# Kernel tuning notes

Hardware: AMD Instinct MI355X
Metric: run time of the kernel (lower is better)

## Reference

```python
import math
import jax, jax.numpy as jnp
import numpy as np

B, L, D, H = 2, 2048, 1024, 16
HD = D // H  # 64

def setup_inputs() -> dict:
    key = jax.random.key(0)
    k1, k2, k3 = jax.random.split(key, 3)
    x = jax.random.normal(k1, (B, L, D), dtype=jnp.float32)
    Wqkv = jax.random.normal(k2, (3 * D, D), dtype=jnp.float32) * (1.0 / math.sqrt(D))
    Wo = jax.random.normal(k3, (D, D), dtype=jnp.float32) * (1.0 / math.sqrt(D))
    return {"x": x, "Wqkv": Wqkv, "Wo": Wo}

def reference(x, Wqkv, Wo):
    # QKV projection (torch Linear: y = x @ W.T), then split
    qkv = jnp.einsum('bld,ed->ble', x, Wqkv)  # [B, L, 3D]
    q, k, v = jnp.split(qkv, 3, axis=-1)
    # [B, H, L, HD]
    q = q.reshape(B, L, H, HD).transpose(0, 2, 1, 3)
    k = k.reshape(B, L, H, HD).transpose(0, 2, 1, 3)
    v = v.reshape(B, L, H, HD).transpose(0, 2, 1, 3)
    # scores; causal mask applied before the 1/sqrt(d) scale (as in source;
    # -inf is unchanged by scaling so math matches scale-then-mask)
    scores = jnp.einsum('bhqd,bhkd->bhqk', q, k)
    causal = jnp.tril(jnp.ones((L, L), dtype=bool))
    scores = jnp.where(causal, scores, -jnp.inf)
    attn = jax.nn.softmax(scores / math.sqrt(HD), axis=-1)
    out = jnp.einsum('bhqk,bhkd->bhqd', attn, v)  # [B, H, L, HD]
    out = out.transpose(0, 2, 1, 3).reshape(B, L, D)
    # output projection (dropout is identity in eval / p=0)
    return jnp.einsum('bld,ed->ble', out, Wo)
```

## Files before the change

kernel.cpp:

```cpp
#include <hip/hip_runtime.h>
#include <hip/hip_bf16.h>
#include <cstdint>
#include <cstddef>

#define B_SZ 2
#define L_SEQ 2048
#define DM 1024
#define NH 16
#define HDIM 64
#define BL (B_SZ * L_SEQ)
#define QKV_N (3 * DM)

typedef __attribute__((ext_vector_type(4))) float f32x4;
typedef __attribute__((ext_vector_type(16))) float f32x16;
typedef __attribute__((ext_vector_type(8))) short bf16x8;
typedef __attribute__((ext_vector_type(2))) unsigned int u32x2;
typedef __attribute__((ext_vector_type(4))) unsigned int u32x4;
typedef unsigned short u16;
typedef __attribute__((ext_vector_type(4))) unsigned short u16x4;

__device__ __forceinline__ float bf2f(u16 u) {
  union { unsigned int i; float f; } c; c.i = ((unsigned int)u) << 16; return c.f;
}
__device__ __forceinline__ u16 f2bf(float f) {
  union { float f; unsigned int i; } c; c.f = f;
  unsigned int r = c.i + 0x7fffu + ((c.i >> 16) & 1u);
  return (u16)(r >> 16);
}

__device__ __forceinline__ void gload_lds16(const void* g, void* l) {
  __builtin_amdgcn_global_load_lds(
      (const __attribute__((address_space(1))) void*)g,
      (__attribute__((address_space(3))) void*)l, 16, 0, 0);
}

__device__ __forceinline__ f32x16 mfma32(bf16x8 a, bf16x8 b, f32x16 c) {
  return __builtin_amdgcn_mfma_f32_32x32x16_bf16(a, b, c, 0, 0, 0);
}

__device__ __forceinline__ unsigned cvtpk(float lo, float hi) {
  unsigned r;
  asm("v_cvt_pk_bf16_f32 %0, %1, %2" : "=v"(r) : "v"(lo), "v"(hi));
  return r;
}
__device__ __forceinline__ void plswap(unsigned& a, unsigned& b) {
  asm("v_permlane32_swap_b32 %0, %1" : "+v"(a), "+v"(b));
}

template <int BASE>
__device__ __forceinline__ bf16x8 pack_bfrag(const f32x16& v) {
  unsigned a  = cvtpk(v[BASE + 0], v[BASE + 1]);
  unsigned a2 = cvtpk(v[BASE + 2], v[BASE + 3]);
  unsigned b  = cvtpk(v[BASE + 4], v[BASE + 5]);
  unsigned b2 = cvtpk(v[BASE + 6], v[BASE + 7]);
  plswap(a, b);
  plswap(a2, b2);
  u32x4 fw; fw[0] = a; fw[1] = a2; fw[2] = b; fw[3] = b2;
  return __builtin_bit_cast(bf16x8, fw);
}

#define N4_X  (BL * DM / 4)
#define N4_WQ (QKV_N * DM / 4)
#define N4_WO (DM * DM / 4)
__global__ __launch_bounds__(256) void cvt_all(
    const float* __restrict__ x, const float* __restrict__ wqkv,
    const float* __restrict__ wo, u16* __restrict__ x_bf,
    u16* __restrict__ w_bf, u16* __restrict__ wo_bf) {
  int i = blockIdx.x * blockDim.x + threadIdx.x;
  const int stride = gridDim.x * blockDim.x;
  const int total = N4_X + N4_WQ + N4_WO;
  for (; i < total; i += stride) {
    const float4* src;
    u16x4* dst;
    if (i < N4_X) {
      src = (const float4*)x + i; dst = (u16x4*)x_bf + i;
    } else if (i < N4_X + N4_WQ) {
      src = (const float4*)wqkv + (i - N4_X); dst = (u16x4*)w_bf + (i - N4_X);
    } else {
      src = (const float4*)wo + (i - N4_X - N4_WQ);
      dst = (u16x4*)wo_bf + (i - N4_X - N4_WQ);
    }
    float4 v = *src;
    u16x4 o;
    o[0] = f2bf(v.x); o[1] = f2bf(v.y); o[2] = f2bf(v.z); o[3] = f2bf(v.w);
    *dst = o;
  }
}

template <bool BF16_OUT>
__global__ __launch_bounds__(256) void gemm_bt(
    const u16* __restrict__ A, const u16* __restrict__ B,
    void* __restrict__ Cv, int M, int N, int K, int nbx) {
  __shared__ u16 As[128 * 64];
  __shared__ u16 Bs[128 * 64];
  const int tid = threadIdx.x;
  const int lane = tid & 63, w = tid >> 6;
  const int l31 = lane & 31, hi = lane >> 5;
  const int wr = w >> 1, wc = w & 1;

  const int bid = (int)blockIdx.x;
  const int swz = (bid & 7) * ((int)gridDim.x >> 3) + (bid >> 3);
  const int bm = (swz / nbx) * 128, bn = (swz % nbx) * 128;

  f32x16 acc00 = {}, acc01 = {}, acc10 = {}, acc11 = {};

  const int srow = lane >> 3;
  const int csw = ((lane & 7) ^ srow) * 8;
  const size_t abase = (size_t)(bm + w * 32 + srow) * K + csw;
  const size_t bbase = (size_t)(bn + w * 32 + srow) * K + csw;
  const int sw = l31 & 7;

  for (int k0 = 0; k0 < K; k0 += 64) {
#pragma unroll
    for (int c = 0; c < 4; ++c)
      gload_lds16(A + abase + (size_t)c * 8 * K + k0, &As[(w * 32 + c * 8) * 64]);
#pragma unroll
    for (int c = 0; c < 4; ++c)
      gload_lds16(B + bbase + (size_t)c * 8 * K + k0, &Bs[(w * 32 + c * 8) * 64]);
    __syncthreads();

#pragma unroll
    for (int ks = 0; ks < 4; ++ks) {
      const int sl = ((ks * 2 + hi) ^ sw) * 8;
      const bf16x8 a0 = *(const bf16x8*)&As[(wr * 64 + l31) * 64 + sl];
      const bf16x8 a1 = *(const bf16x8*)&As[(wr * 64 + 32 + l31) * 64 + sl];
      const bf16x8 b0 = *(const bf16x8*)&Bs[(wc * 64 + l31) * 64 + sl];
      const bf16x8 b1 = *(const bf16x8*)&Bs[(wc * 64 + 32 + l31) * 64 + sl];
      acc00 = mfma32(a0, b0, acc00);
      acc01 = mfma32(a0, b1, acc01);
      acc10 = mfma32(a1, b0, acc10);
      acc11 = mfma32(a1, b1, acc11);
    }
    __syncthreads();
  }

#define CWRITE(ACC, MI, NI)                                                    \
  {                                                                            \
    _Pragma("unroll")                                                          \
    for (int r = 0; r < 16; ++r) {                                             \
      const int row = bm + wr * 64 + (MI)*32 + (r & 3) + 8 * (r >> 2) + 4 * hi;\
      const int col = bn + wc * 64 + (NI)*32 + l31;                            \
      if (BF16_OUT)                                                            \
        ((u16*)Cv)[(size_t)row * N + col] = f2bf(ACC[r]);                      \
      else                                                                     \
        ((float*)Cv)[(size_t)row * N + col] = ACC[r];                          \
    }                                                                          \
  }
  CWRITE(acc00, 0, 0)
  CWRITE(acc01, 0, 1)
  CWRITE(acc10, 1, 0)
  CWRITE(acc11, 1, 1)
#undef CWRITE
}

__device__ const uint8_t JST[20] = {7,7,7,7, 6,6,6, 5,5,5, 4,4, 3,3, 2, 1,
                                    6, 4, 2, 0};
__device__ const uint8_t JT0[20] = {0,8,16,24, 0,8,16, 0,8,16, 0,8, 0,8, 0, 0,
                                    24, 16, 8, 0};
__device__ const uint8_t JT1[20] = {8,16,24,32, 8,16,24, 8,16,24, 8,16, 8,16, 8, 8,
                                    28, 20, 12, 4};
__device__ const uint8_t SB[8]   = {255, 255, 0, 2, 4, 7, 10, 14};
__device__ const uint8_t SCNT[8] = {1, 1, 2, 2, 3, 3, 4, 4};

__global__ __launch_bounds__(512) void attn_fused(const u16* __restrict__ qkv,
                                                  u16* __restrict__ aout,
                                                  u16* __restrict__ opart_lo,
                                                  u16* __restrict__ opart_hi,
                                                  float* __restrict__ lpart) {
  __shared__ u16 Kl[2][64 * 64];
  __shared__ u16 Vt[2][64 * 64];

  const int tid = threadIdx.x;
  const int lane = tid & 63, w = tid >> 6;
  const int l31 = lane & 31, hi = lane >> 5;
  const int id = (int)blockIdx.x;
  const int bh = id & 31, j = id >> 5;
  const int st = JST[j];
  const int t0 = JT0[j], t1 = JT1[j];
  const int b = bh >> 4, h = bh & 15;
  const u16* base = qkv + (size_t)b * L_SEQ * QKV_N;
  const int W = st * 256 + w * 32;
  const int qrow = W + l31;

  const int krow = tid >> 3;
  const int ks = tid & 7;
  const int kr7 = krow & 7;
  const u16* gpk_base = base + (size_t)krow * QKV_N + DM + h * HDIM + ks * 8;
  bf16x8 kr;

  const int vd0 = (tid & 31) * 2;
  const int vkg = tid >> 5;
  const int vge = tid & 7;
  const int vgo = (tid & 7) ^ 4;
  const u16* gpv_base = base + (size_t)(vkg * 4) * QKV_N + 2 * DM + h * HDIM + vd0;
  unsigned int vtmp[4];

  auto issue_loads = [&](int t) {
    kr = *(const bf16x8*)(gpk_base + (size_t)t * 64 * QKV_N);
    const u16* gpv = gpv_base + (size_t)t * 64 * QKV_N;
#pragma unroll
    for (int jj = 0; jj < 4; ++jj)
      vtmp[jj] = *(const unsigned int*)(gpv + (size_t)jj * QKV_N);
  };
  auto write_lds = [&](int buf) {
    *(bf16x8*)&Kl[buf][krow * 64 + ((ks ^ kr7) * 8)] = kr;
    u32x2 lo, hiw;
    lo[0]  = __builtin_amdgcn_perm(vtmp[1], vtmp[0], 0x05040100u);
    lo[1]  = __builtin_amdgcn_perm(vtmp[3], vtmp[2], 0x05040100u);
    hiw[0] = __builtin_amdgcn_perm(vtmp[1], vtmp[0], 0x07060302u);
    hiw[1] = __builtin_amdgcn_perm(vtmp[3], vtmp[2], 0x07060302u);
    *(u32x2*)&Vt[buf][vd0 * 64 + (((vkg >> 1) ^ vge) * 8) + (vkg & 1) * 4] = lo;
    *(u32x2*)&Vt[buf][(vd0 + 1) * 64 + (((vkg >> 1) ^ vgo) * 8) + (vkg & 1) * 4] = hiw;
  };

  bf16x8 bq[4];
  {
    const u16* qp = base + (size_t)qrow * QKV_N + h * HDIM + hi * 8;
#pragma unroll
    for (int dc = 0; dc < 4; ++dc) {
      bf16x8 tq = *(const bf16x8*)(qp + dc * 16);
#pragma unroll
      for (int i = 0; i < 8; ++i)
        tq[i] = (short)f2bf(bf2f((u16)tq[i]) * 0.18033688f);
      bq[dc] = tq;
    }
  }

  f32x16 acc0 = {}, acc1 = {};
  float lrow = 0.f;

  const int vg = ((l31 >> 1) & 7) ^ ((l31 & 1) << 2);
  const int lsw = l31 & 7;

  issue_loads(t0);
  write_lds(0);
  __syncthreads();

  for (int t = t0; t < t1; ++t) {
    const int cur = (t - t0) & 1;
    if (t + 1 < t1) issue_loads(t + 1);

    if (64 * t <= W + 31) {
      f32x16 s0 = {}, s1 = {};
#pragma unroll
      for (int dc = 0; dc < 4; ++dc) {
        const int sl = ((dc * 2 + hi) ^ lsw) * 8;
        const bf16x8 k0 = *(const bf16x8*)&Kl[cur][l31 * 64 + sl];
        const bf16x8 k1 = *(const bf16x8*)&Kl[cur][(32 + l31) * 64 + sl];
        s0 = mfma32(k0, bq[dc], s0);
        s1 = mfma32(k1, bq[dc], s1);
      }

      if (64 * t + 63 > W) {
#pragma unroll
        for (int r = 0; r < 16; ++r) {
          const int kg = t * 64 + (r & 3) + 8 * (r >> 2) + 4 * hi;
          if (kg > qrow) s0[r] = -1e30f;
          if (kg + 32 > qrow) s1[r] = -1e30f;
        }
      }

#pragma unroll
      for (int r = 0; r < 16; ++r) {
        s0[r] = exp2f(s0[r]);
        s1[r] = exp2f(s1[r]);
      }
      float r0 = 0.f, r1 = 0.f, r2 = 0.f, r3 = 0.f;
#pragma unroll
      for (int r = 0; r < 16; r += 4) {
        r0 += s0[r] + s0[r + 1];
        r1 += s0[r + 2] + s0[r + 3];
        r2 += s1[r] + s1[r + 1];
        r3 += s1[r + 2] + s1[r + 3];
      }
      lrow += (r0 + r1) + (r2 + r3);

      const bf16x8 pf0 = pack_bfrag<0>(s0);
      const bf16x8 pf1 = pack_bfrag<8>(s0);
      const bf16x8 pf2 = pack_bfrag<0>(s1);
      const bf16x8 pf3 = pack_bfrag<8>(s1);

#pragma unroll
      for (int c = 0; c < 4; ++c) {
        const bf16x8 pf = c == 0 ? pf0 : c == 1 ? pf1 : c == 2 ? pf2 : pf3;
        const int sl = ((c * 2 + hi) ^ vg) * 8;
        const bf16x8 va = *(const bf16x8*)&Vt[cur][l31 * 64 + sl];
        const bf16x8 vb = *(const bf16x8*)&Vt[cur][(32 + l31) * 64 + sl];
        acc0 = mfma32(va, pf, acc0);
        acc1 = mfma32(vb, pf, acc1);
      }
    }

    if (t + 1 < t1) write_lds(((t + 1) - t0) & 1);
    __syncthreads();
  }

  lrow += __shfl_xor(lrow, 32);

  if (SB[st] != 255) {
    const int c = t0 >> 3;
    const int slot = ((int)SB[st] + c) * 32 + bh;
    u16* po = slot < 512 ? opart_lo + (size_t)slot * 16384
                         : opart_hi + (size_t)(slot - 512) * 16384;
    const int q = w * 32 + l31;
#pragma unroll
    for (int i = 0; i < 16; ++i) {
      const int d0 = (i & 3) + 8 * (i >> 2) + 4 * hi;
      po[d0 * 256 + q] = f2bf(acc0[i]);
      po[(d0 + 32) * 256 + q] = f2bf(acc1[i]);
    }
    if (hi == 0) lpart[slot * 256 + q] = lrow;
  } else {
    const float inv = 1.f / lrow;
#pragma unroll
    for (int i = 0; i < 16; ++i) { acc0[i] *= inv; acc1[i] *= inv; }
    const bf16x8 of0 = pack_bfrag<0>(acc0);
    const bf16x8 of1 = pack_bfrag<8>(acc0);
    const bf16x8 of2 = pack_bfrag<0>(acc1);
    const bf16x8 of3 = pack_bfrag<8>(acc1);
    u16* op = aout + (size_t)(b * L_SEQ + qrow) * DM + h * HDIM + hi * 8;
    *(bf16x8*)(op + 0)  = of0;
    *(bf16x8*)(op + 16) = of1;
    *(bf16x8*)(op + 32) = of2;
    *(bf16x8*)(op + 48) = of3;
  }
}

__global__ __launch_bounds__(256) void attn_combine(
    const u16* __restrict__ opart_lo, const u16* __restrict__ opart_hi,
    const float* __restrict__ lpart, u16* __restrict__ aout) {
  const int gid = (int)blockIdx.x * 256 + (int)threadIdx.x;
  const int q = gid & 255;
  const int u = gid >> 8;
  const int st = 2 + (u >> 5), bh = u & 31;
  const int b = bh >> 4, h = bh & 15;
  const int nc = (int)SCNT[st];
  const int sb = (int)SB[st];

  const u16* pp[4];
  float L = 0.f;
#pragma unroll
  for (int c = 0; c < 4; ++c)
    if (c < nc) {
      const int slot = (sb + c) * 32 + bh;
      L += lpart[slot * 256 + q];
      pp[c] = slot < 512 ? opart_lo + (size_t)slot * 16384
                         : opart_hi + (size_t)(slot - 512) * 16384;
    }
  const float invl = 1.f / L;

  const int qrow = st * 256 + q;
  u16* op = aout + (size_t)(b * L_SEQ + qrow) * DM + h * HDIM;
#pragma unroll
  for (int d0 = 0; d0 < 64; d0 += 8) {
    float v[8] = {};
#pragma unroll
    for (int c = 0; c < 4; ++c)
      if (c < nc) {
#pragma unroll
        for (int jj = 0; jj < 8; ++jj)
          v[jj] += bf2f(pp[c][(d0 + jj) * 256 + q]);
      }
    u16x4 oa, ob;
#pragma unroll
    for (int jj = 0; jj < 4; ++jj) {
      oa[jj] = f2bf(v[jj] * invl);
      ob[jj] = f2bf(v[jj + 4] * invl);
    }
    *(u16x4*)(op + d0) = oa;
    *(u16x4*)(op + d0 + 4) = ob;
  }
}

extern "C" void kernel_launch(void* const* d_in, const int* in_sizes, int n_in,
                              void* d_out, int out_size, void* d_ws, size_t ws_size,
                              hipStream_t stream) {
  (void)in_sizes; (void)n_in; (void)out_size; (void)ws_size;
  const float* x = (const float*)d_in[0];
  const float* wqkv = (const float*)d_in[1];
  const float* wo = (const float*)d_in[2];

  char* ws = (char*)d_ws;
  u16* x_bf = (u16*)(ws);
  u16* w_bf = (u16*)(ws + (size_t)(8u << 20));
  u16* wo_bf = (u16*)(ws + (size_t)(14u << 20));
  u16* qkv_bf = (u16*)(ws + (size_t)(16u << 20));
  u16* ao_bf = x_bf;
  u16* opart_lo = (u16*)d_out;
  u16* opart_hi = (u16*)(ws + (size_t)(8u << 20));
  float* lpart = (float*)(ws + (size_t)(10u << 20));

  cvt_all<<<2048, 256, 0, stream>>>(x, wqkv, wo, x_bf, w_bf, wo_bf);

  gemm_bt<true><<<dim3(768), 256, 0, stream>>>(x_bf, w_bf, (void*)qkv_bf,
                                               BL, QKV_N, DM, QKV_N / 128);

  attn_fused<<<dim3(640), 512, 0, stream>>>(qkv_bf, ao_bf, opart_lo, opart_hi, lpart);
  attn_combine<<<dim3(192), 256, 0, stream>>>(opart_lo, opart_hi, lpart, ao_bf);

  gemm_bt<false><<<dim3(256), 256, 0, stream>>>(ao_bf, wo_bf, d_out,
                                                BL, DM, DM, DM / 128);
}
```

Measured before the change: 124.3 us.

## Fuse split-KV combine into attention kernel via last-block atomic counter

Removes the separate attn_combine launch and instead has the last finishing split block for each (stripe, head) combine the partial outputs, using a global atomic counter and threadfences. This aims to save a kernel launch and its tail latency. In exchange it adds a memset launch, extra syncthreads and fences in every split block, and a serialized combine tail run by one block per group.

Measured after the change: 260.5 us. 2.1x slower.

```diff
diff --git a/kernel.cpp b/kernel.cpp
--- a/kernel.cpp
+++ b/kernel.cpp
@@ -166,9 +166,11 @@
                                                   u16* __restrict__ aout,
                                                   u16* __restrict__ opart_lo,
                                                   u16* __restrict__ opart_hi,
-                                                  float* __restrict__ lpart) {
+                                                  float* __restrict__ lpart,
+                                                  int* __restrict__ cnt) {
   __shared__ u16 Kl[2][64 * 64];
   __shared__ u16 Vt[2][64 * 64];
+  __shared__ int lastFlag;
 
   const int tid = threadIdx.x;
   const int lane = tid & 63, w = tid >> 6;
@@ -299,7 +301,9 @@
 
   if (SB[st] != 255) {
     const int c = t0 >> 3;
-    const int slot = ((int)SB[st] + c) * 32 + bh;
+    const int sb = (int)SB[st];
+    const int nc = (int)SCNT[st];
+    const int slot = (sb + c) * 32 + bh;
     u16* po = slot < 512 ? opart_lo + (size_t)slot * 16384
                          : opart_hi + (size_t)(slot - 512) * 16384;
     const int q = w * 32 + l31;
@@ -310,6 +314,52 @@
       po[(d0 + 32) * 256 + q] = f2bf(acc1[i]);
     }
     if (hi == 0) lpart[slot * 256 + q] = lrow;
+
+    __syncthreads();
+    __threadfence();
+    __syncthreads();
+    if (tid == 0) {
+      const int old = atomicAdd(&cnt[(st - 2) * 32 + bh], 1);
+      lastFlag = (old == nc - 1);
+    }
+    __syncthreads();
+    if (lastFlag) {
+      __threadfence();
+      const int cq = tid & 255;
+      const int dh = tid >> 8;
+      const u16* pp[4];
+      float L = 0.f;
+#pragma unroll
+      for (int cc = 0; cc < 4; ++cc)
+        if (cc < nc) {
+          const int s2 = (sb + cc) * 32 + bh;
+          L += lpart[s2 * 256 + cq];
+          pp[cc] = s2 < 512 ? opart_lo + (size_t)s2 * 16384
+                            : opart_hi + (size_t)(s2 - 512) * 16384;
+        }
+      const float invl = 1.f / L;
+      const int qr2 = st * 256 + cq;
+      u16* op = aout + (size_t)(b * L_SEQ + qr2) * DM + h * HDIM + dh * 32;
+#pragma unroll
+      for (int d0 = 0; d0 < 32; d0 += 8) {
+        float v[8] = {};
+#pragma unroll
+        for (int cc = 0; cc < 4; ++cc)
+          if (cc < nc) {
+#pragma unroll
+            for (int jj = 0; jj < 8; ++jj)
+              v[jj] += bf2f(pp[cc][(dh * 32 + d0 + jj) * 256 + cq]);
+          }
+        u16x4 oa, ob;
+#pragma unroll
+        for (int jj = 0; jj < 4; ++jj) {
+          oa[jj] = f2bf(v[jj] * invl);
+          ob[jj] = f2bf(v[jj + 4] * invl);
+        }
+        *(u16x4*)(op + d0) = oa;
+        *(u16x4*)(op + d0 + 4) = ob;
+      }
+    }
   } else {
     const float inv = 1.f / lrow;
 #pragma unroll
@@ -326,52 +376,6 @@
   }
 }
 
-__global__ __launch_bounds__(256) void attn_combine(
-    const u16* __restrict__ opart_lo, const u16* __restrict__ opart_hi,
-    const float* __restrict__ lpart, u16* __restrict__ aout) {
-  const int gid = (int)blockIdx.x * 256 + (int)threadIdx.x;
-  const int q = gid & 255;
-  const int u = gid >> 8;
-  const int st = 2 + (u >> 5), bh = u & 31;
-  const int b = bh >> 4, h = bh & 15;
-  const int nc = (int)SCNT[st];
-  const int sb = (int)SB[st];
-
-  const u16* pp[4];
-  float L = 0.f;
-#pragma unroll
-  for (int c = 0; c < 4; ++c)
-    if (c < nc) {
-      const int slot = (sb + c) * 32 + bh;
-      L += lpart[slot * 256 + q];
-      pp[c] = slot < 512 ? opart_lo + (size_t)slot * 16384
-                         : opart_hi + (size_t)(slot - 512) * 16384;
-    }
-  const float invl = 1.f / L;
-
-  const int qrow = st * 256 + q;
-  u16* op = aout + (size_t)(b * L_SEQ + qrow) * DM + h * HDIM;
-#pragma unroll
-  for (int d0 = 0; d0 < 64; d0 += 8) {
-    float v[8] = {};
-#pragma unroll
-    for (int c = 0; c < 4; ++c)
-      if (c < nc) {
-#pragma unroll
-        for (int jj = 0; jj < 8; ++jj)
-          v[jj] += bf2f(pp[c][(d0 + jj) * 256 + q]);
-      }
-    u16x4 oa, ob;
-#pragma unroll
-    for (int jj = 0; jj < 4; ++jj) {
-      oa[jj] = f2bf(v[jj] * invl);
-      ob[jj] = f2bf(v[jj + 4] * invl);
-    }
-    *(u16x4*)(op + d0) = oa;
-    *(u16x4*)(op + d0 + 4) = ob;
-  }
-}
-
 extern "C" void kernel_launch(void* const* d_in, const int* in_sizes, int n_in,
                               void* d_out, int out_size, void* d_ws, size_t ws_size,
                               hipStream_t stream) {
@@ -389,14 +393,17 @@
   u16* opart_lo = (u16*)d_out;
   u16* opart_hi = (u16*)(ws + (size_t)(8u << 20));
   float* lpart = (float*)(ws + (size_t)(10u << 20));
+  int* cnt = (int*)(ws + (size_t)(11u << 20));
 
   cvt_all<<<2048, 256, 0, stream>>>(x, wqkv, wo, x_bf, w_bf, wo_bf);
 
   gemm_bt<true><<<dim3(768), 256, 0, stream>>>(x_bf, w_bf, (void*)qkv_bf,
                                                BL, QKV_N, DM, QKV_N / 128);
 
-  attn_fused<<<dim3(640), 512, 0, stream>>>(qkv_bf, ao_bf, opart_lo, opart_hi, lpart);
-  attn_combine<<<dim3(192), 256, 0, stream>>>(opart_lo, opart_hi, lpart, ao_bf);
+  hipMemsetAsync(cnt, 0, 192 * sizeof(int), stream);
+
+  attn_fused<<<dim3(640), 512, 0, stream>>>(qkv_bf, ao_bf, opart_lo, opart_hi,
+                                            lpart, cnt);
 
   gemm_bt<false><<<dim3(256), 256, 0, stream>>>(ao_bf, wo_bf, d_out,
                                                 BL, DM, DM, DM / 128);
```

## Double-buffer GEMM LDS tiles with K-step 32 to overlap loads with MFMA

Applied to the files above, without the earlier changes.

Changes the GEMM main loop from a single 128x64 LDS tile per operand to two 128x32 buffers. The next K-slice is issued with direct global-to-LDS loads while MFMAs run on the current buffer. The XOR swizzle is adapted to the narrower rows. This aims to hide global load latency behind compute, at the cost of twice as many loop iterations and barriers per K. It also depends on correct barrier placement between the buffers, which is not fully visible here.

Result: slower. 130.1 us (+4.6%).

```diff
diff --git a/kernel.cpp b/kernel.cpp
--- a/kernel.cpp
+++ b/kernel.cpp
@@ -91,8 +91,8 @@
 __global__ __launch_bounds__(256) void gemm_bt(
     const u16* __restrict__ A, const u16* __restrict__ B,
     void* __restrict__ Cv, int M, int N, int K, int nbx) {
-  __shared__ u16 As[128 * 64];
-  __shared__ u16 Bs[128 * 64];
+  __shared__ u16 As[2][128 * 32];
+  __shared__ u16 Bs[2][128 * 32];
   const int tid = threadIdx.x;
   const int lane = tid & 63, w = tid >> 6;
   const int l31 = lane & 31, hi = lane >> 5;
@@ -104,28 +104,33 @@
 
   f32x16 acc00 = {}, acc01 = {}, acc10 = {}, acc11 = {};
 
-  const int srow = lane >> 3;
-  const int csw = ((lane & 7) ^ srow) * 8;
+  const int srow = lane >> 2;
+  const int csw = ((lane & 3) ^ ((lane >> 3) & 3)) * 8;
   const size_t abase = (size_t)(bm + w * 32 + srow) * K + csw;
   const size_t bbase = (size_t)(bn + w * 32 + srow) * K + csw;
-  const int sw = l31 & 7;
-
-  for (int k0 = 0; k0 < K; k0 += 64) {
-#pragma unroll
-    for (int c = 0; c < 4; ++c)
-      gload_lds16(A + abase + (size_t)c * 8 * K + k0, &As[(w * 32 + c * 8) * 64]);
-#pragma unroll
-    for (int c = 0; c < 4; ++c)
-      gload_lds16(B + bbase + (size_t)c * 8 * K + k0, &Bs[(w * 32 + c * 8) * 64]);
-    __syncthreads();
-
-#pragma unroll
-    for (int ks = 0; ks < 4; ++ks) {
-      const int sl = ((ks * 2 + hi) ^ sw) * 8;
-      const bf16x8 a0 = *(const bf16x8*)&As[(wr * 64 + l31) * 64 + sl];
-      const bf16x8 a1 = *(const bf16x8*)&As[(wr * 64 + 32 + l31) * 64 + sl];
-      const bf16x8 b0 = *(const bf16x8*)&Bs[(wc * 64 + l31) * 64 + sl];
-      const bf16x8 b1 = *(const bf16x8*)&Bs[(wc * 64 + 32 + l31) * 64 + sl];
+  const int sw = (l31 >> 1) & 3;
+
+  auto stage = [&](int buf, int k0) {
+    gload_lds16(A + abase + k0,                 &As[buf][(w * 32) * 32]);
+    gload_lds16(A + abase + (size_t)16 * K + k0, &As[buf][(w * 32 + 16) * 32]);
+    gload_lds16(B + bbase + k0,                 &Bs[buf][(w * 32) * 32]);
+    gload_lds16(B + bbase + (size_t)16 * K + k0, &Bs[buf][(w * 32 + 16) * 32]);
+  };
+
+  stage(0, 0);
+  __syncthreads();
+
+  for (int k0 = 0; k0 < K; k0 += 32) {
+    const int buf = (k0 >> 5) & 1;
+    if (k0 + 32 < K) stage(buf ^ 1, k0 + 32);
+
+#pragma unroll
+    for (int kk = 0; kk < 2; ++kk) {
+      const int sl = ((kk * 2 + hi) ^ sw) * 8;
+      const bf16x8 a0 = *(const bf16x8*)&As[buf][(wr * 64 + l31) * 32 + sl];
+      const bf16x8 a1 = *(const bf16x8*)&As[buf][(wr * 64 + 32 + l31) * 32 + sl];
+      const bf16x8 b0 = *(const bf16x8*)&Bs[buf][(wc * 64 + l31) * 32 + sl];
+      const bf16x8 b1 = *(const bf16x8*)&Bs[buf][(wc * 64 + 32 + l31) * 32 + sl];
       acc00 = mfma32(a0, b0, acc00);
       acc01 = mfma32(a0, b1, acc01);
       acc10 = mfma32(a1, b0, acc10);
```

## Stage K via direct global-to-LDS loads, deepen V prefetch, compute row sums with MFMA

Applied to the files above, without the earlier changes.

K tiles are now copied straight from global memory into LDS with a direct-to-LDS load, replacing the register round trip. V loads are prefetched two tiles ahead, and each V tile is written into the other LDS buffer at the start of the iteration instead of the end. The softmax row sums are no longer taken with scalar adds and a cross-lane shuffle; an extra MFMA against a vector of ones accumulates them. This shortens the per-iteration scalar/VALU path and overlaps memory with compute, at the cost of one more MFMA per chunk and extra accumulator registers, which may reduce occupancy.

After: 126.2 us. No clear change (+1.5%).

```diff
diff --git a/kernel.cpp b/kernel.cpp
--- a/kernel.cpp
+++ b/kernel.cpp
@@ -182,11 +182,11 @@
   const int W = st * 256 + w * 32;
   const int qrow = W + l31;
 
-  const int krow = tid >> 3;
-  const int ks = tid & 7;
-  const int kr7 = krow & 7;
-  const u16* gpk_base = base + (size_t)krow * QKV_N + DM + h * HDIM + ks * 8;
-  bf16x8 kr;
+  const u16* kf_src = base + (size_t)(w * 8 + (lane >> 3)) * QKV_N + DM +
+                      h * HDIM + (((lane & 7) ^ (lane >> 3)) * 8);
+  auto stage_K = [&](int t, int buf) {
+    gload_lds16(kf_src + (size_t)t * 64 * QKV_N, &Kl[buf][w * 512]);
+  };
 
   const int vd0 = (tid & 31) * 2;
   const int vkg = tid >> 5;
@@ -195,15 +195,13 @@
   const u16* gpv_base = base + (size_t)(vkg * 4) * QKV_N + 2 * DM + h * HDIM + vd0;
   unsigned int vtmp[4];
 
-  auto issue_loads = [&](int t) {
-    kr = *(const bf16x8*)(gpk_base + (size_t)t * 64 * QKV_N);
+  auto issue_V = [&](int t) {
     const u16* gpv = gpv_base + (size_t)t * 64 * QKV_N;
 #pragma unroll
     for (int jj = 0; jj < 4; ++jj)
       vtmp[jj] = *(const unsigned int*)(gpv + (size_t)jj * QKV_N);
   };
-  auto write_lds = [&](int buf) {
-    *(bf16x8*)&Kl[buf][krow * 64 + ((ks ^ kr7) * 8)] = kr;
+  auto write_V = [&](int buf) {
     u32x2 lo, hiw;
     lo[0]  = __builtin_amdgcn_perm(vtmp[1], vtmp[0], 0x05040100u);
     lo[1]  = __builtin_amdgcn_perm(vtmp[3], vtmp[2], 0x05040100u);
@@ -226,19 +224,29 @@
     }
   }
 
+  bf16x8 ones;
+#pragma unroll
+  for (int i = 0; i < 8; ++i) ones[i] = (short)0x3F80;
+
   f32x16 acc0 = {}, acc1 = {};
-  float lrow = 0.f;
+  f32x16 acc2 = {};
 
   const int vg = ((l31 >> 1) & 7) ^ ((l31 & 1) << 2);
   const int lsw = l31 & 7;
 
-  issue_loads(t0);
-  write_lds(0);
+  stage_K(t0, 0);
+  issue_V(t0);
+  write_V(0);
+  issue_V(t0 + 1);
   __syncthreads();
 
   for (int t = t0; t < t1; ++t) {
     const int cur = (t - t0) & 1;
-    if (t + 1 < t1) issue_loads(t + 1);
+    if (t + 1 < t1) {
+      write_V(cur ^ 1);
+      stage_K(t + 1, cur ^ 1);
+    }
+    if (t + 2 < t1) issue_V(t + 2);
 
     if (64 * t <= W + 31) {
       f32x16 s0 = {}, s1 = {};
@@ -265,15 +273,6 @@
         s0[r] = exp2f(s0[r]);
         s1[r] = exp2f(s1[r]);
       }
-      float r0 = 0.f, r1 = 0.f, r2 = 0.f, r3 = 0.f;
-#pragma unroll
-      for (int r = 0; r < 16; r += 4) {
-        r0 += s0[r] + s0[r + 1];
-        r1 += s0[r + 2] + s0[r + 3];
-        r2 += s1[r] + s1[r + 1];
-        r3 += s1[r + 2] + s1[r + 3];
-      }
-      lrow += (r0 + r1) + (r2 + r3);
 
       const bf16x8 pf0 = pack_bfrag<0>(s0);
       const bf16x8 pf1 = pack_bfrag<8>(s0);
@@ -288,14 +287,14 @@
         const bf16x8 vb = *(const bf16x8*)&Vt[cur][(32 + l31) * 64 + sl];
         acc0 = mfma32(va, pf, acc0);
         acc1 = mfma32(vb, pf, acc1);
+        acc2 = mfma32(ones, pf, acc2);
       }
     }
 
-    if (t + 1 < t1) write_lds(((t + 1) - t0) & 1);
     __syncthreads();
   }
 
-  lrow += __shfl_xor(lrow, 32);
+  const float lrow = acc2[0];
 
   if (SB[st] != 255) {
     const int c = t0 >> 3;
```
